# Optimization experiments

Hardware: AMD Instinct MI355X
Metric: run time of the kernel (lower is better)

Reference implementation:

```python
import jax, jax.numpy as jnp
import numpy as np

N_PIXELS = 262144  # 512x512 FOV
N_COMP = 1000      # neuron components (columns of sparse A)
NNZ = 400000       # ~400 nonzero pixels per component
N_BG = 2           # dense background columns
BATCH = 128


def setup_inputs() -> dict:
    key = jax.random.key(0)
    k0, k1, k2, k3, k4 = jax.random.split(key, 5)
    X = jax.random.normal(k0, (BATCH, N_PIXELS), dtype=jnp.float32)
    A_rows = jax.random.randint(k1, (NNZ,), 0, N_PIXELS, dtype=jnp.int32)
    A_cols = jax.random.randint(k2, (NNZ,), 0, N_COMP, dtype=jnp.int32)
    A_vals = jax.random.normal(k3, (NNZ,), dtype=jnp.float32)
    b = jax.random.normal(k4, (N_PIXELS, N_BG), dtype=jnp.float32)
    n_AtA = jnp.float32(1000.0)  # Frobenius norm of Ab.T @ Ab (constant scalar)
    return {"X": X, "A_vals": A_vals, "b": b, "n_AtA": n_AtA,
            "A_rows": A_rows, "A_cols": A_cols}


def reference(X, A_vals, b, n_AtA, A_rows, A_cols):
    # Sparse A^T @ X^T in COO form: gather pixel rows of X, scale by values,
    # segment-sum into component rows. data: [nnz, batch]
    data = X[:, A_rows].T * A_vals[:, None]
    Y = jax.ops.segment_sum(data, A_cols, num_segments=N_COMP)  # [n_comp, batch]
    # Dense background term: b^T @ X^T -> [n_bg, batch]
    Y1 = jnp.einsum('pg,bp->gb', b, X)
    Y = jnp.concatenate([Y, Y1], axis=0) / n_AtA
    return Y
```

## Files before the change

kernel.cpp:

```cpp
#include <hip/hip_runtime.h>
#include <hip/hip_bf16.h>

typedef unsigned short u16;
typedef unsigned int   u32;

#define N_PIXELS 262144
#define N_COMP   1000
#define NNZ      400000
#define N_BG     2
#define BATCH    128

#define CAP        576
#define TP_PIX     64
#define TSTRIDE    129
#define SC_BLOCKS  64
#define SC_EPB     (NNZ / SC_BLOCKS)
#define TP_BLOCKS  (N_PIXELS / TP_PIX)
#define HALF_MAX   ((CAP + 1) / 2)
#define BG_BLOCKS  256
#define BG_PPB     (N_PIXELS / BG_BLOCKS)

#define SWZ(b) ((b) ^ ((((b) >> 5) & 3) << 3))

#define WS_CNT    0
#define WS_SLOTS  4096
#define WS_XT     (WS_SLOTS + (size_t)N_COMP * CAP * 8)
#define WS_NEED   (WS_XT + (size_t)N_PIXELS * BATCH * 2)

__device__ __forceinline__ float bflo(u32 w) { return __uint_as_float(w << 16); }
__device__ __forceinline__ float bfhi(u32 w) { return __uint_as_float(w & 0xffff0000u); }


__global__ __launch_bounds__(256) void stage_kernel(
    const float* __restrict__ X,
    const int*   __restrict__ rows, const int* __restrict__ cols,
    const float* __restrict__ vals, const float* __restrict__ nAtA,
    int* __restrict__ cnts, int2* __restrict__ slots,
    u32* __restrict__ XT32)
{
    __shared__ float smem[TP_PIX * TSTRIDE];
    const int tid = threadIdx.x;

    if (blockIdx.x < SC_BLOCKS) {
        int* hist = (int*)smem;
        int* base = hist + N_COMP;
        for (int i = tid; i < N_COMP; i += 256) hist[i] = 0;
        __syncthreads();

        const int e0 = blockIdx.x * SC_EPB;
        for (int j = e0 + tid; j < e0 + SC_EPB; j += 256)
            atomicAdd(&hist[cols[j]], 1);
        __syncthreads();

        for (int c = tid; c < N_COMP; c += 256) {
            const int n = hist[c];
            if (n) base[c] = atomicAdd(&cnts[c], n);
            hist[c] = 0;
        }
        __syncthreads();

        const float inv = 1.0f / nAtA[0];
        for (int j = e0 + tid; j < e0 + SC_EPB; j += 256) {
            const int c = cols[j];
            const int pos = base[c] + atomicAdd(&hist[c], 1);
            if (pos < CAP) {
                int2 e; e.x = rows[j]; e.y = __float_as_int(vals[j] * inv);
                slots[(size_t)c * CAP + pos] = e;
            }
        }
    } else {
        const int p0   = (blockIdx.x - SC_BLOCKS) * TP_PIX;
        const int k    = tid & 15;
        const int rsub = tid >> 4;
#pragma unroll
        for (int pass = 0; pass < 8; ++pass) {
            const int b  = pass * 16 + rsub;
            const float4 x = *(const float4*)(X + (size_t)b * N_PIXELS + p0 + 4 * k);
            const int bs = SWZ(b);
            smem[(4 * k + 0) * TSTRIDE + bs] = x.x;
            smem[(4 * k + 1) * TSTRIDE + bs] = x.y;
            smem[(4 * k + 2) * TSTRIDE + bs] = x.z;
            smem[(4 * k + 3) * TSTRIDE + bs] = x.w;
        }
        __syncthreads();

        const int p  = tid >> 2;
        const int j0 = (tid & 3) * 32;
        const int sj = ((j0 >> 5) & 3) << 3;
        const float* row = smem + p * TSTRIDE + j0;
        u32 out[16];
#pragma unroll
        for (int q = 0; q < 16; ++q) {
            const float lo = row[(2 * q)     ^ sj];
            const float hi = row[(2 * q + 1) ^ sj];
            __hip_bfloat162 h2 = __float22bfloat162_rn(make_float2(lo, hi));
            u32 w; __builtin_memcpy(&w, &h2, 4);
            out[q] = w;
        }
        uint4* dst = (uint4*)(XT32 + (size_t)(p0 + p) * 64 + (j0 >> 1));
#pragma unroll
        for (int q = 0; q < 4; ++q)
            dst[q] = make_uint4(out[4 * q], out[4 * q + 1], out[4 * q + 2], out[4 * q + 3]);
    }
}

__global__ __launch_bounds__(256) void compute_kernel(
    const uint4* __restrict__ XP4,
    const int*   __restrict__ cnts,
    const int2*  __restrict__ slots,
    const float* __restrict__ bmat,
    const float* __restrict__ nAtA,
    float* __restrict__ Y)
{
    __shared__ char smem_raw[12544];
    const int tid  = threadIdx.x;
    const int wave = tid >> 6;
    const int lane = tid & 63;
    const int g    = tid >> 4;
    const int s    = tid & 15;
    const int blk  = blockIdx.x;

    if (blk < 2 * N_COMP) {
        const int comp = blk >> 1;
        const int half = blk & 1;

        int*   sro = (int*)smem_raw;
        float* svv = (float*)(sro + HALF_MAX);
        float* red = (float*)(svv + HALF_MAX);

        int cnt = cnts[comp]; if (cnt > CAP) cnt = CAP;
        const int n0  = (cnt + 1) >> 1;
        const int beg = half ? n0 : 0;
        const int n   = (half ? cnt : n0) - beg;
        const int n_pad = (n + 15) & ~15;

        const int2* sl = slots + (size_t)comp * CAP + beg;
        for (int i = tid; i < n_pad; i += 256) {
            int r = 0; float v = 0.0f;
            if (i < n) { const int2 e = sl[i]; r = e.x; v = __int_as_float(e.y); }
            sro[i] = r << 4;
            svv[i] = v;
        }
        __syncthreads();

        float acc[8] = {0, 0, 0, 0, 0, 0, 0, 0};
#pragma unroll 2
        for (int i = 0; i < n_pad; i += 16) {
            const int   e = i + g;
            const float v = svv[e];
            const uint4 x = XP4[sro[e] + s];
            acc[0] += v * bflo(x.x); acc[1] += v * bfhi(x.x);
            acc[2] += v * bflo(x.y); acc[3] += v * bfhi(x.y);
            acc[4] += v * bflo(x.z); acc[5] += v * bfhi(x.z);
            acc[6] += v * bflo(x.w); acc[7] += v * bfhi(x.w);
        }
#pragma unroll
        for (int m = 16; m <= 32; m <<= 1)
#pragma unroll
            for (int q = 0; q < 8; ++q) acc[q] += __shfl_xor(acc[q], m, 64);
        if (lane < 16)
#pragma unroll
            for (int q = 0; q < 8; ++q) red[wave * 128 + lane * 8 + q] = acc[q];
        __syncthreads();
        if (tid < 128) {
            const float r0 = red[tid] + red[128 + tid] + red[256 + tid] + red[384 + tid];
            atomicAdd(&Y[(size_t)comp * BATCH + tid], r0);
        }
    } else {
        float2* bb   = (float2*)smem_raw;
        float*  red0 = (float*)(bb + BG_PPB);
        float*  red1 = red0 + 512;

        const int p0 = (blk - 2 * N_COMP) * BG_PPB;
        const float2* bm2 = (const float2*)bmat;
        for (int i = tid; i < BG_PPB; i += 256) bb[i] = bm2[p0 + i];
        __syncthreads();

        float a0[8] = {0,0,0,0,0,0,0,0}, a1[8] = {0,0,0,0,0,0,0,0};
#pragma unroll 2
        for (int i = g; i < BG_PPB; i += 16) {
            const uint4  x  = XP4[(size_t)(p0 + i) * 16 + s];
            const float2 b2 = bb[i];
            const float f0 = bflo(x.x), f1 = bfhi(x.x), f2 = bflo(x.y), f3 = bfhi(x.y);
            const float f4 = bflo(x.z), f5 = bfhi(x.z), f6 = bflo(x.w), f7 = bfhi(x.w);
            a0[0] += b2.x * f0; a0[1] += b2.x * f1; a0[2] += b2.x * f2; a0[3] += b2.x * f3;
            a0[4] += b2.x * f4; a0[5] += b2.x * f5; a0[6] += b2.x * f6; a0[7] += b2.x * f7;
            a1[0] += b2.y * f0; a1[1] += b2.y * f1; a1[2] += b2.y * f2; a1[3] += b2.y * f3;
            a1[4] += b2.y * f4; a1[5] += b2.y * f5; a1[6] += b2.y * f6; a1[7] += b2.y * f7;
        }
#pragma unroll
        for (int m = 16; m <= 32; m <<= 1)
#pragma unroll
            for (int q = 0; q < 8; ++q) {
                a0[q] += __shfl_xor(a0[q], m, 64);
                a1[q] += __shfl_xor(a1[q], m, 64);
            }
        if (lane < 16)
#pragma unroll
            for (int q = 0; q < 8; ++q) {
                red0[wave * 128 + lane * 8 + q] = a0[q];
                red1[wave * 128 + lane * 8 + q] = a1[q];
            }
        __syncthreads();
        if (tid < 128) {
            const float inv = 1.0f / nAtA[0];
            float* Ybg = Y + (size_t)N_COMP * BATCH;
            const float r0 = red0[tid] + red0[128 + tid] + red0[256 + tid] + red0[384 + tid];
            const float r1 = red1[tid] + red1[128 + tid] + red1[256 + tid] + red1[384 + tid];
            atomicAdd(&Ybg[tid],         r0 * inv);
            atomicAdd(&Ybg[BATCH + tid], r1 * inv);
        }
    }
}


#define NB          8
#define NNZ_CHUNKS  64
#define CHUNK_SZ    ((NNZ + NNZ_CHUNKS - 1) / NNZ_CHUNKS)

__global__ __launch_bounds__(256) void fb_hist_kernel(
    const float* __restrict__ X, const float* __restrict__ vals,
    const int* __restrict__ rows, const int* __restrict__ cols,
    const float* __restrict__ nAtA, float* __restrict__ Y)
{
    __shared__ float hist[NB * N_COMP];
    const int tid = threadIdx.x, chunk = blockIdx.x, b0 = blockIdx.y * NB;
    for (int i = tid; i < NB * N_COMP; i += 256) hist[i] = 0.0f;
    __syncthreads();
    const float inv = 1.0f / nAtA[0];
    const int e0 = chunk * CHUNK_SZ;
    const int e1 = (e0 + CHUNK_SZ < NNZ) ? (e0 + CHUNK_SZ) : NNZ;
    const float* Xb = X + (size_t)b0 * N_PIXELS;
    for (int j = e0 + tid; j < e1; j += 256) {
        const int r = rows[j], c = cols[j];
        const float v = vals[j] * inv;
        float x[NB];
#pragma unroll
        for (int k = 0; k < NB; ++k) x[k] = Xb[(size_t)k * N_PIXELS + r];
#pragma unroll
        for (int k = 0; k < NB; ++k) atomicAdd(&hist[k * N_COMP + c], v * x[k]);
    }
    __syncthreads();
    for (int i = tid; i < N_COMP * NB; i += 256) {
        const int c = i >> 3, k = i & 7;
        atomicAdd(&Y[(size_t)c * BATCH + b0 + k], hist[k * N_COMP + c]);
    }
}

__global__ __launch_bounds__(256) void fb_bg_kernel(
    const float* __restrict__ X, const float* __restrict__ bmat,
    const float* __restrict__ nAtA, float* __restrict__ Y)
{
    const int b = blockIdx.x, chunk = blockIdx.y, tid = threadIdx.x;
    const int p0 = chunk * (N_PIXELS / 8);
    const float4* X4 = (const float4*)(X + (size_t)b * N_PIXELS + p0);
    const float4* B4 = (const float4*)(bmat + (size_t)p0 * N_BG);
    float s0 = 0.0f, s1 = 0.0f;
    for (int i = tid; i < (N_PIXELS / 8) / 4; i += 256) {
        const float4 x = X4[i];
        const float4 g0 = B4[2 * i], g1 = B4[2 * i + 1];
        s0 += x.x * g0.x + x.y * g0.z + x.z * g1.x + x.w * g1.z;
        s1 += x.x * g0.y + x.y * g0.w + x.z * g1.y + x.w * g1.w;
    }
#pragma unroll
    for (int off = 32; off > 0; off >>= 1) {
        s0 += __shfl_down(s0, off, 64);
        s1 += __shfl_down(s1, off, 64);
    }
    if ((tid & 63) == 0) {
        const float inv = 1.0f / nAtA[0];
        atomicAdd(&Y[(size_t)N_COMP * BATCH + b],       s0 * inv);
        atomicAdd(&Y[(size_t)(N_COMP + 1) * BATCH + b], s1 * inv);
    }
}


extern "C" void kernel_launch(void* const* d_in, const int* in_sizes, int n_in,
                              void* d_out, int out_size, void* d_ws, size_t ws_size,
                              hipStream_t stream) {
    const float* X     = (const float*)d_in[0];
    const float* Avals = (const float*)d_in[1];
    const float* bmat  = (const float*)d_in[2];
    const float* nAtA  = (const float*)d_in[3];
    const int*   Arows = (const int*)d_in[4];
    const int*   Acols = (const int*)d_in[5];
    float*       Y     = (float*)d_out;

    if (ws_size >= WS_NEED) {
        char* ws = (char*)d_ws;
        int*  cnts  = (int*)(ws + WS_CNT);
        int2* slots = (int2*)(ws + WS_SLOTS);
        u32*  XT32  = (u32*)(ws + WS_XT);

        hipMemsetAsync(cnts, 0, 4096, stream);
        hipMemsetAsync(d_out, 0, (size_t)out_size * sizeof(float), stream);

        stage_kernel<<<SC_BLOCKS + TP_BLOCKS, 256, 0, stream>>>(
            X, Arows, Acols, Avals, nAtA, cnts, slots, XT32);
        compute_kernel<<<2 * N_COMP + BG_BLOCKS, 256, 0, stream>>>(
            (const uint4*)XT32, cnts, slots, bmat, nAtA, Y);
    } else {
        hipMemsetAsync(d_out, 0, (size_t)out_size * sizeof(float), stream);
        dim3 sgrid(NNZ_CHUNKS, BATCH / NB);
        fb_hist_kernel<<<sgrid, 256, 0, stream>>>(X, Avals, Arows, Acols, nAtA, Y);
        dim3 bgrid(BATCH, 8);
        fb_bg_kernel<<<bgrid, 256, 0, stream>>>(X, bmat, nAtA, Y);
    }
}
```

Before: 273.7 us.

## Shrink transpose tile, use float4 swizzled LDS writes, pad atomic counters

The transpose stage now uses 32-pixel tiles stored batch-major with an XOR swizzle on float4 groups, so LDS writes are 128-bit and reads stride down columns. The block count doubles and an occupancy hint of 8 blocks per CU is added. Per-component counters are padded to 16 ints apart so the global atomics land on separate cache lines, and the memset grows to match. This aims to cut LDS bank conflicts and atomic contention, at the cost of more blocks and a larger counter memset.

Result: no change. 270.5 us (-1.2%).

```diff
diff --git a/kernel.cpp b/kernel.cpp
--- a/kernel.cpp
+++ b/kernel.cpp
@@ -11,8 +11,8 @@
 #define BATCH    128
 
 #define CAP        576
-#define TP_PIX     64
-#define TSTRIDE    129
+#define TP_PIX     32
+#define TS         36
 #define SC_BLOCKS  64
 #define SC_EPB     (NNZ / SC_BLOCKS)
 #define TP_BLOCKS  (N_PIXELS / TP_PIX)
@@ -20,10 +20,10 @@
 #define BG_BLOCKS  256
 #define BG_PPB     (N_PIXELS / BG_BLOCKS)
 
-#define SWZ(b) ((b) ^ ((((b) >> 5) & 3) << 3))
+#define CNT_PAD 16
 
 #define WS_CNT    0
-#define WS_SLOTS  4096
+#define WS_SLOTS  65536
 #define WS_XT     (WS_SLOTS + (size_t)N_COMP * CAP * 8)
 #define WS_NEED   (WS_XT + (size_t)N_PIXELS * BATCH * 2)
 
@@ -31,14 +31,14 @@
 __device__ __forceinline__ float bfhi(u32 w) { return __uint_as_float(w & 0xffff0000u); }
 
 
-__global__ __launch_bounds__(256) void stage_kernel(
+__global__ __launch_bounds__(256, 8) void stage_kernel(
     const float* __restrict__ X,
     const int*   __restrict__ rows, const int* __restrict__ cols,
     const float* __restrict__ vals, const float* __restrict__ nAtA,
     int* __restrict__ cnts, int2* __restrict__ slots,
     u32* __restrict__ XT32)
 {
-    __shared__ float smem[TP_PIX * TSTRIDE];
+    __shared__ float smem[BATCH * TS];
     const int tid = threadIdx.x;
 
     if (blockIdx.x < SC_BLOCKS) {
@@ -54,7 +54,7 @@
 
         for (int c = tid; c < N_COMP; c += 256) {
             const int n = hist[c];
-            if (n) base[c] = atomicAdd(&cnts[c], n);
+            if (n) base[c] = atomicAdd(&cnts[c * CNT_PAD], n);
             hist[c] = 0;
         }
         __syncthreads();
@@ -69,40 +69,38 @@
             }
         }
     } else {
-        const int p0   = (blockIdx.x - SC_BLOCKS) * TP_PIX;
-        const int k    = tid & 15;
-        const int rsub = tid >> 4;
-#pragma unroll
-        for (int pass = 0; pass < 8; ++pass) {
-            const int b  = pass * 16 + rsub;
+        const int p0 = (blockIdx.x - SC_BLOCKS) * TP_PIX;
+        const int k  = tid & 7;
+        const int bq = tid >> 3;
+#pragma unroll
+        for (int pass = 0; pass < 4; ++pass) {
+            const int b = pass * 32 + bq;
             const float4 x = *(const float4*)(X + (size_t)b * N_PIXELS + p0 + 4 * k);
-            const int bs = SWZ(b);
-            smem[(4 * k + 0) * TSTRIDE + bs] = x.x;
-            smem[(4 * k + 1) * TSTRIDE + bs] = x.y;
-            smem[(4 * k + 2) * TSTRIDE + bs] = x.z;
-            smem[(4 * k + 3) * TSTRIDE + bs] = x.w;
-        }
-        __syncthreads();
-
-        const int p  = tid >> 2;
-        const int j0 = (tid & 3) * 32;
-        const int sj = ((j0 >> 5) & 3) << 3;
-        const float* row = smem + p * TSTRIDE + j0;
-        u32 out[16];
-#pragma unroll
-        for (int q = 0; q < 16; ++q) {
-            const float lo = row[(2 * q)     ^ sj];
-            const float hi = row[(2 * q + 1) ^ sj];
+            const int m = (b >> 4) & 7;
+            *(float4*)&smem[b * TS + 4 * (k ^ m)] = x;
+        }
+        __syncthreads();
+
+        const int p    = tid >> 3;
+        const int j0   = (tid & 7) * 16;
+        const int m    = (j0 >> 4) & 7;
+        const int slot = 4 * ((p >> 2) ^ m) + (p & 3);
+        const float* col = smem + slot;
+        u32 out[8];
+#pragma unroll
+        for (int q = 0; q < 8; ++q) {
+            const float lo = col[(j0 + 2 * q)     * TS];
+            const float hi = col[(j0 + 2 * q + 1) * TS];
             __hip_bfloat162 h2 = __float22bfloat162_rn(make_float2(lo, hi));
             u32 w; __builtin_memcpy(&w, &h2, 4);
             out[q] = w;
         }
         uint4* dst = (uint4*)(XT32 + (size_t)(p0 + p) * 64 + (j0 >> 1));
-#pragma unroll
-        for (int q = 0; q < 4; ++q)
-            dst[q] = make_uint4(out[4 * q], out[4 * q + 1], out[4 * q + 2], out[4 * q + 3]);
-    }
-}
+        dst[0] = make_uint4(out[0], out[1], out[2], out[3]);
+        dst[1] = make_uint4(out[4], out[5], out[6], out[7]);
+    }
+}
+
 
 __global__ __launch_bounds__(256) void compute_kernel(
     const uint4* __restrict__ XP4,
@@ -128,7 +126,7 @@
         float* svv = (float*)(sro + HALF_MAX);
         float* red = (float*)(svv + HALF_MAX);
 
-        int cnt = cnts[comp]; if (cnt > CAP) cnt = CAP;
+        int cnt = cnts[comp * CNT_PAD]; if (cnt > CAP) cnt = CAP;
         const int n0  = (cnt + 1) >> 1;
         const int beg = half ? n0 : 0;
         const int n   = (half ? cnt : n0) - beg;
@@ -292,7 +290,7 @@
         int2* slots = (int2*)(ws + WS_SLOTS);
         u32*  XT32  = (u32*)(ws + WS_XT);
 
-        hipMemsetAsync(cnts, 0, 4096, stream);
+        hipMemsetAsync(cnts, 0, 65536, stream);
         hipMemsetAsync(d_out, 0, (size_t)out_size * sizeof(float), stream);
 
         stage_kernel<<<SC_BLOCKS + TP_BLOCKS, 256, 0, stream>>>(
```
